# Kernel optimization log

Hardware: AMD Instinct MI355X
Metric: run time of the kernel (lower is better)

## Reference

```python
import jax, jax.numpy as jnp
import numpy as np

N_NODES = 100_000
N_EDGES = 4_000_000


def setup_inputs() -> dict:
    key = jax.random.key(0)
    k1, k2, k3, k4 = jax.random.split(key, 4)
    frac_coords = jax.random.uniform(k1, (N_NODES, 3), dtype=jnp.float32)
    edge_indices = jax.random.randint(k2, (2, N_EDGES), 0, N_NODES, dtype=jnp.int32)
    symmops = jax.random.normal(k3, (N_EDGES, 4, 4), dtype=jnp.float32)
    cell_translations = jax.random.normal(k4, (N_EDGES, 3), dtype=jnp.float32)
    return {
        "frac_coords": frac_coords,
        "edge_indices": edge_indices,
        "symmops": symmops,
        "cell_translations": cell_translations,
    }


def reference(frac_coords, edge_indices, symmops, cell_translations):
    # Gather node positions for each edge (NodePosition with selection_index [0, 1]).
    in_frac = frac_coords[edge_indices[0]]   # (M, 3)
    out_frac = frac_coords[edge_indices[1]]  # (M, 3)
    # Homogeneous coordinate: (M, 4)
    out_h = jnp.concatenate([out_frac, jnp.ones_like(out_frac[:, :1])], axis=1)
    # Per-edge 4x4 affine transform, keep first 3 components.
    out_t = jnp.einsum('ij,ikj->ik', out_h, symmops)[:, :3]
    # Periodic wrap into [0, 1) then shift by cell translation.
    out_t = out_t - jnp.floor(out_t) + cell_translations
    # Displacement vector per edge.
    return in_frac - out_t
```

## Files before the change

### kernel.cpp

```cpp
#include <hip/hip_runtime.h>


typedef float vf4 __attribute__((ext_vector_type(4)));

__global__ __launch_bounds__(256) void pad_frac_kernel(
    const float* __restrict__ frac, vf4* __restrict__ fracp, int N)
{
    int i = blockIdx.x * blockDim.x + threadIdx.x;
    if (i < N) {
        vf4 v;
        v.x = frac[3 * i + 0];
        v.y = frac[3 * i + 1];
        v.z = frac[3 * i + 2];
        v.w = 0.0f;
        fracp[i] = v;
    }
}

__global__ __launch_bounds__(256) void disp_vec_main(
    const vf4*   __restrict__ fracp,
    const int*   __restrict__ eidx,
    const float* __restrict__ symm,
    const float* __restrict__ ct,
    float*       __restrict__ out,
    int M)
{
    __shared__ float lds[768];
    const int tid  = threadIdx.x;
    const int base = blockIdx.x * 256;
    const int i    = base + tid;

    if (tid < 192) {
        const vf4* c4 = (const vf4*)(ct + (size_t)base * 3);
        ((vf4*)lds)[tid] = __builtin_nontemporal_load(c4 + tid);
    }

    const int n0 = __builtin_nontemporal_load(eidx + i);
    const int n1 = __builtin_nontemporal_load(eidx + M + i);

    const vf4* s = (const vf4*)(symm + (size_t)i * 16);
    const vf4 r0 = __builtin_nontemporal_load(s + 0);
    const vf4 r1 = __builtin_nontemporal_load(s + 1);
    const vf4 r2 = __builtin_nontemporal_load(s + 2);

    const vf4 fin = fracp[n0];
    const vf4 fo  = fracp[n1];

    float t0 = fo.x * r0.x + fo.y * r0.y + fo.z * r0.z + r0.w;
    float t1 = fo.x * r1.x + fo.y * r1.y + fo.z * r1.z + r1.w;
    float t2 = fo.x * r2.x + fo.y * r2.y + fo.z * r2.z + r2.w;

    t0 -= floorf(t0);
    t1 -= floorf(t1);
    t2 -= floorf(t2);

    __syncthreads();
    const float c0 = lds[3 * tid + 0];
    const float c1 = lds[3 * tid + 1];
    const float c2 = lds[3 * tid + 2];

    const float o0 = fin.x - (t0 + c0);
    const float o1 = fin.y - (t1 + c1);
    const float o2 = fin.z - (t2 + c2);

    __syncthreads();
    lds[3 * tid + 0] = o0;
    lds[3 * tid + 1] = o1;
    lds[3 * tid + 2] = o2;
    __syncthreads();

    if (tid < 192) {
        vf4* o4 = (vf4*)(out + (size_t)base * 3);
        __builtin_nontemporal_store(((vf4*)lds)[tid], o4 + tid);
    }
    (void)M;
}

__global__ __launch_bounds__(256) void disp_vec_scalar(
    const float* __restrict__ frac,
    const int*   __restrict__ eidx,
    const float* __restrict__ symm,
    const float* __restrict__ ct,
    float*       __restrict__ out,
    int M, int start)
{
    int i = start + blockIdx.x * blockDim.x + threadIdx.x;
    if (i >= M) return;

    int n0 = eidx[i];
    int n1 = eidx[M + i];

    const float* f0 = frac + (size_t)n0 * 3;
    const float* f1 = frac + (size_t)n1 * 3;

    const float4* s = (const float4*)(symm + (size_t)i * 16);
    float4 r0 = s[0], r1 = s[1], r2 = s[2];

    float ox = f1[0], oy = f1[1], oz = f1[2];
    float t0 = ox * r0.x + oy * r0.y + oz * r0.z + r0.w;
    float t1 = ox * r1.x + oy * r1.y + oz * r1.z + r1.w;
    float t2 = ox * r2.x + oy * r2.y + oz * r2.z + r2.w;

    t0 -= floorf(t0);
    t1 -= floorf(t1);
    t2 -= floorf(t2);

    const float* c = ct + (size_t)i * 3;
    float* o = out + (size_t)i * 3;
    o[0] = f0[0] - (t0 + c[0]);
    o[1] = f0[1] - (t1 + c[1]);
    o[2] = f0[2] - (t2 + c[2]);
}

extern "C" void kernel_launch(void* const* d_in, const int* in_sizes, int n_in,
                              void* d_out, int out_size, void* d_ws, size_t ws_size,
                              hipStream_t stream) {
    const float* frac = (const float*)d_in[0];
    const int*   eidx = (const int*)d_in[1];
    const float* symm = (const float*)d_in[2];
    const float* ct   = (const float*)d_in[3];
    float* out = (float*)d_out;

    const int N = in_sizes[0] / 3;
    const int M = in_sizes[1] / 2;

    const size_t need = (size_t)N * sizeof(vf4);
    if (ws_size >= need) {
        vf4* fracp = (vf4*)d_ws;
        pad_frac_kernel<<<(N + 255) / 256, 256, 0, stream>>>(frac, fracp, N);

        const int full_tiles = M / 256;
        const int rem        = M % 256;
        if (full_tiles > 0) {
            disp_vec_main<<<full_tiles, 256, 0, stream>>>(fracp, eidx, symm, ct, out, M);
        }
        if (rem > 0) {
            disp_vec_scalar<<<1, 256, 0, stream>>>(frac, eidx, symm, ct, out, M, full_tiles * 256);
        }
    } else {
        disp_vec_scalar<<<(M + 255) / 256, 256, 0, stream>>>(frac, eidx, symm, ct, out, M, 0);
    }
}
```

Baseline: 433.9 us.

## Stage symmop matrices through padded LDS with fully coalesced loads

Each block now loads its whole 256x4x4 symmop tile with contiguous vf4 loads, including the unused fourth row, into shared memory padded to avoid bank conflicts. Each thread then reads its three needed rows from LDS. Cell translations are read directly per thread instead of through LDS, and the nontemporal load hints are dropped. The aim is fully coalesced global reads in place of strided 48-of-64-byte per-thread reads, at the cost of fetching the fourth row, more LDS traffic and a barrier before compute.

```diff
diff --git a/kernel.cpp b/kernel.cpp
--- a/kernel.cpp
+++ b/kernel.cpp
@@ -25,26 +25,35 @@
     float*       __restrict__ out,
     int M)
 {
-    __shared__ float lds[768];
+    __shared__ vf4   sy[1152];
+    __shared__ float so[768];
+
     const int tid  = threadIdx.x;
     const int base = blockIdx.x * 256;
     const int i    = base + tid;
 
-    if (tid < 192) {
-        const vf4* c4 = (const vf4*)(ct + (size_t)base * 3);
-        ((vf4*)lds)[tid] = __builtin_nontemporal_load(c4 + tid);
+    const vf4* sg = (const vf4*)(symm + (size_t)base * 16);
+    #pragma unroll
+    for (int k = 0; k < 4; ++k) {
+        const int slot = k * 256 + tid;
+        sy[slot + (slot >> 3)] = sg[slot];
     }
 
-    const int n0 = __builtin_nontemporal_load(eidx + i);
-    const int n1 = __builtin_nontemporal_load(eidx + M + i);
-
-    const vf4* s = (const vf4*)(symm + (size_t)i * 16);
-    const vf4 r0 = __builtin_nontemporal_load(s + 0);
-    const vf4 r1 = __builtin_nontemporal_load(s + 1);
-    const vf4 r2 = __builtin_nontemporal_load(s + 2);
+    const int n0 = eidx[i];
+    const int n1 = eidx[M + i];
+    const float c0 = ct[3 * (size_t)i + 0];
+    const float c1 = ct[3 * (size_t)i + 1];
+    const float c2 = ct[3 * (size_t)i + 2];
 
     const vf4 fin = fracp[n0];
     const vf4 fo  = fracp[n1];
+
+    __syncthreads();
+
+    const int s0 = 4 * tid;
+    const vf4 r0 = sy[s0     + ((s0    ) >> 3)];
+    const vf4 r1 = sy[s0 + 1 + ((s0 + 1) >> 3)];
+    const vf4 r2 = sy[s0 + 2 + ((s0 + 2) >> 3)];
 
     float t0 = fo.x * r0.x + fo.y * r0.y + fo.z * r0.z + r0.w;
     float t1 = fo.x * r1.x + fo.y * r1.y + fo.z * r1.z + r1.w;
@@ -54,24 +63,14 @@
     t1 -= floorf(t1);
     t2 -= floorf(t2);
 
-    __syncthreads();
-    const float c0 = lds[3 * tid + 0];
-    const float c1 = lds[3 * tid + 1];
-    const float c2 = lds[3 * tid + 2];
-
-    const float o0 = fin.x - (t0 + c0);
-    const float o1 = fin.y - (t1 + c1);
-    const float o2 = fin.z - (t2 + c2);
-
-    __syncthreads();
-    lds[3 * tid + 0] = o0;
-    lds[3 * tid + 1] = o1;
-    lds[3 * tid + 2] = o2;
+    so[3 * tid + 0] = fin.x - (t0 + c0);
+    so[3 * tid + 1] = fin.y - (t1 + c1);
+    so[3 * tid + 2] = fin.z - (t2 + c2);
     __syncthreads();
 
     if (tid < 192) {
         vf4* o4 = (vf4*)(out + (size_t)base * 3);
-        __builtin_nontemporal_store(((vf4*)lds)[tid], o4 + tid);
+        __builtin_nontemporal_store(((vf4*)so)[tid], o4 + tid);
     }
     (void)M;
 }
```

New measurement: 418.1 us. 1.04x faster.
